# Kernel tuning notes

Hardware: AMD Instinct MI355X
Metric: run time of the kernel (lower is better)

The kernel has to match this reference:

```python
import jax, jax.numpy as jnp
import numpy as np

N_IN = 200000
N_OUT = 400000
K = 27          # 3x3x3 kernel offsets
P = 100000      # rulebook pairs per offset
C_IN = 32
C_OUT = 32


def setup_inputs() -> dict:
    key = jax.random.key(0)
    k1, k2, k3, k4, k5 = jax.random.split(key, 5)
    feats = jax.random.normal(k1, (N_IN, C_IN), dtype=jnp.float32)
    weight = jax.random.normal(k2, (K, C_IN, C_OUT), dtype=jnp.float32) * (1.0 / np.sqrt(C_IN * K))
    bias_param = jax.random.normal(k3, (C_OUT,), dtype=jnp.float32) * 0.01
    pairs_in = jax.random.randint(k4, (K, P), 0, N_IN, dtype=jnp.int64)
    pairs_out = jax.random.randint(k5, (K, P), 0, N_OUT, dtype=jnp.int64)
    return {
        "feats": feats,
        "weight": weight,
        "bias_param": bias_param,
        "pairs_in": pairs_in,
        "pairs_out": pairs_out,
        "n_out": N_OUT,
    }


def reference(feats, weight, bias_param, pairs_in, pairs_out, n_out):
    # Rulebook-based sparse inverse conv3d:
    #   1) gather input features per kernel offset  -> [K, P, C_in]
    #   2) per-offset GEMM with that offset's slice -> [K, P, C_out]
    #   3) scatter-add results into output voxels   -> [N_out, C_out]
    gathered = feats[pairs_in]                       # [K, P, C_in]
    vals = jnp.einsum('kpc,kco->kpo', gathered, weight)  # [K, P, C_out]
    out = jnp.zeros((n_out, vals.shape[-1]), dtype=feats.dtype)
    out = out.at[pairs_out.reshape(-1)].add(vals.reshape(-1, vals.shape[-1]))
    out = out + bias_param
    return out
```

## Files before the change

### kernel.cpp

```cpp
#include <hip/hip_runtime.h>

#define KK 27
#define PP 100000
#define C_IN 32
#define C_OUT 32
#define N_IN 200000
#define N_OUT 400000
#define PAIRS_PER_BLOCK 160

__global__ __launch_bounds__(256) void init_out_kernel(
    float4* __restrict__ out4, const float4* __restrict__ bias4) {
    int i = blockIdx.x * 256 + threadIdx.x;
    out4[i] = bias4[i & 7];
}

__global__ __launch_bounds__(256) void spconv_scatter_kernel(
    const float* __restrict__ feats,
    const float* __restrict__ weight,
    const int* __restrict__ pin,
    const int* __restrict__ pout,
    float* __restrict__ out)
{
    const int k   = blockIdx.y;
    const int c   = threadIdx.x & 31;
    const int grp = threadIdx.x >> 5;

    const float* w = weight + k * (C_IN * C_OUT) + c;
    float wcol[C_IN];
#pragma unroll
    for (int ci = 0; ci < C_IN; ++ci) wcol[ci] = w[ci * C_OUT];

    const int* pin_k  = pin  + k * PP;
    const int* pout_k = pout + k * PP;

    const int base = blockIdx.x * PAIRS_PER_BLOCK + grp;

#pragma unroll 4
    for (int i = 0; i < PAIRS_PER_BLOCK / 8; ++i) {
        const int p  = base + i * 8;
        const int ii = pin_k[p];
        const int io = pout_k[p];

        const float4* f4 = (const float4*)(feats + ii * 32);
        float acc = 0.0f;
#pragma unroll
        for (int j = 0; j < 8; ++j) {
            const float4 f = f4[j];
            acc = fmaf(f.x, wcol[4 * j + 0], acc);
            acc = fmaf(f.y, wcol[4 * j + 1], acc);
            acc = fmaf(f.z, wcol[4 * j + 2], acc);
            acc = fmaf(f.w, wcol[4 * j + 3], acc);
        }
        atomicAdd(out + io * 32 + c, acc);
    }
}

extern "C" void kernel_launch(void* const* d_in, const int* in_sizes, int n_in,
                              void* d_out, int out_size, void* d_ws, size_t ws_size,
                              hipStream_t stream) {
    const float* feats  = (const float*)d_in[0];
    const float* weight = (const float*)d_in[1];
    const float* bias   = (const float*)d_in[2];
    const int*   pin    = (const int*)d_in[3];
    const int*   pout   = (const int*)d_in[4];
    float*       out    = (float*)d_out;

    const int n_f4 = N_OUT * C_OUT / 4;
    init_out_kernel<<<n_f4 / 256, 256, 0, stream>>>(
        (float4*)out, (const float4*)bias);

    dim3 grid(PP / PAIRS_PER_BLOCK, KK);
    spconv_scatter_kernel<<<grid, 256, 0, stream>>>(
        feats, weight, pin, pout, out);
}
```

Baseline: 497.0 us.

## Partition output rows into XCD-local slices to localize scatter atomics

Each block now scans a chunk of pairs and processes only those whose output row falls in one of 16 row slices. Blocks are ordered so that round-robin dispatch sends each slice to a fixed XCD, keeping the atomic targets inside that XCD's L2. The change also switches to unsafeAtomicAdd, which lets the compiler emit hardware float atomics, and uses nontemporal loads for indices and features. The cost is that every pout index is read 16 times and the per-pair branch diverges within a wave.

Result: slower. 1.227 ms (+147.0%).

```diff
diff --git a/kernel.cpp b/kernel.cpp
--- a/kernel.cpp
+++ b/kernel.cpp
@@ -6,22 +6,40 @@
 #define C_OUT 32
 #define N_IN 200000
 #define N_OUT 400000
-#define PAIRS_PER_BLOCK 160
+
+#define SLICES 16
+#define ROWS_PER_SLICE (N_OUT / SLICES)
+#define XCDS 8
+#define CHUNK 4000
+#define CGRPS (PP / CHUNK)
+#define HALF_BLOCKS (XCDS * CGRPS * KK)
+#define TOTAL_BLOCKS (2 * HALF_BLOCKS)
+
+typedef int   vint4   __attribute__((ext_vector_type(4)));
+typedef float vfloat4 __attribute__((ext_vector_type(4)));
 
 __global__ __launch_bounds__(256) void init_out_kernel(
-    float4* __restrict__ out4, const float4* __restrict__ bias4) {
+    vfloat4* __restrict__ out4, const vfloat4* __restrict__ bias4) {
     int i = blockIdx.x * 256 + threadIdx.x;
     out4[i] = bias4[i & 7];
 }
 
-__global__ __launch_bounds__(256) void spconv_scatter_kernel(
+__global__ __launch_bounds__(256) void spconv_sliced_kernel(
     const float* __restrict__ feats,
     const float* __restrict__ weight,
     const int* __restrict__ pin,
     const int* __restrict__ pout,
     float* __restrict__ out)
 {
-    const int k   = blockIdx.y;
+    const int b    = blockIdx.x;
+    const int sub  = b / HALF_BLOCKS;
+    const int bb   = b % HALF_BLOCKS;
+    const int xslc = bb % XCDS;
+    const int rest = bb / XCDS;
+    const int cgrp = rest % CGRPS;
+    const int k    = rest / CGRPS;
+    const int r_lo = (xslc + XCDS * sub) * ROWS_PER_SLICE;
+
     const int c   = threadIdx.x & 31;
     const int grp = threadIdx.x >> 5;
 
@@ -33,25 +51,31 @@
     const int* pin_k  = pin  + k * PP;
     const int* pout_k = pout + k * PP;
 
-    const int base = blockIdx.x * PAIRS_PER_BLOCK + grp;
+    const int span = cgrp * CHUNK + grp * (CHUNK / 8);
+    const vint4* po4p = (const vint4*)(pout_k + span);
 
-#pragma unroll 4
-    for (int i = 0; i < PAIRS_PER_BLOCK / 8; ++i) {
-        const int p  = base + i * 8;
-        const int ii = pin_k[p];
-        const int io = pout_k[p];
+    for (int i4 = 0; i4 < CHUNK / 8 / 4; ++i4) {
+        const vint4 po4 = __builtin_nontemporal_load(po4p + i4);
+#pragma unroll
+        for (int j = 0; j < 4; ++j) {
+            const int io = po4[j];
+            if ((unsigned)(io - r_lo) < (unsigned)ROWS_PER_SLICE) {
+                const int p  = span + i4 * 4 + j;
+                const int ii = __builtin_nontemporal_load(pin_k + p);
 
-        const float4* f4 = (const float4*)(feats + ii * 32);
-        float acc = 0.0f;
+                const vfloat4* f4 = (const vfloat4*)(feats + ii * 32);
+                float acc = 0.0f;
 #pragma unroll
-        for (int j = 0; j < 8; ++j) {
-            const float4 f = f4[j];
-            acc = fmaf(f.x, wcol[4 * j + 0], acc);
-            acc = fmaf(f.y, wcol[4 * j + 1], acc);
-            acc = fmaf(f.z, wcol[4 * j + 2], acc);
-            acc = fmaf(f.w, wcol[4 * j + 3], acc);
+                for (int q = 0; q < 8; ++q) {
+                    const vfloat4 f = __builtin_nontemporal_load(f4 + q);
+                    acc = fmaf(f.x, wcol[4 * q + 0], acc);
+                    acc = fmaf(f.y, wcol[4 * q + 1], acc);
+                    acc = fmaf(f.z, wcol[4 * q + 2], acc);
+                    acc = fmaf(f.w, wcol[4 * q + 3], acc);
+                }
+                unsafeAtomicAdd(out + io * 32 + c, acc);
+            }
         }
-        atomicAdd(out + io * 32 + c, acc);
     }
 }
 
@@ -67,9 +91,8 @@
 
     const int n_f4 = N_OUT * C_OUT / 4;
     init_out_kernel<<<n_f4 / 256, 256, 0, stream>>>(
-        (float4*)out, (const float4*)bias);
+        (vfloat4*)out, (const vfloat4*)bias);
 
-    dim3 grid(PP / PAIRS_PER_BLOCK, KK);
-    spconv_scatter_kernel<<<grid, 256, 0, stream>>>(
+    spconv_sliced_kernel<<<TOTAL_BLOCKS, 256, 0, stream>>>(
         feats, weight, pin, pout, out);
 }
```

## Bucket rulebook pairs by output row block and accumulate in shared memory

Applied to the files above, without the earlier changes.

Replaces the global-atomic scatter with a counting-sort of all rulebook pairs into buckets of 128 output rows (count, column scan, base scan, scatter), then one block per bucket gathers features, applies the per-offset weights, accumulates with shared-memory atomics and writes each output row once with bias added. This removes global atomic traffic and the separate output init pass. In exchange it adds four preprocessing kernels with their own passes over the index arrays, a serial column-scan kernel, a single-block scan, and weight reloads whenever the offset changes within a bucket. Pair order inside a bucket is nondeterministic, so offsets may interleave and force frequent weight reloads.

New measurement: 643.1 us. 1.29x slower.

```diff
diff --git a/kernel.cpp b/kernel.cpp
--- a/kernel.cpp
+++ b/kernel.cpp
@@ -2,56 +2,196 @@
 
 #define KK 27
 #define PP 100000
+#define RTOT (KK * PP)
 #define C_IN 32
 #define C_OUT 32
 #define N_IN 200000
 #define N_OUT 400000
-#define PAIRS_PER_BLOCK 160
-
-__global__ __launch_bounds__(256) void init_out_kernel(
-    float4* __restrict__ out4, const float4* __restrict__ bias4) {
-    int i = blockIdx.x * 256 + threadIdx.x;
-    out4[i] = bias4[i & 7];
-}
-
-__global__ __launch_bounds__(256) void spconv_scatter_kernel(
+
+#define RPB 128
+#define NBUCK (N_OUT / RPB)
+#define NBLKA 450
+#define CHA (RTOT / NBLKA)
+
+typedef float vfloat4 __attribute__((ext_vector_type(4)));
+
+
+__global__ __launch_bounds__(256) void countA_kernel(
+    const int* __restrict__ pout, unsigned* __restrict__ C) {
+    __shared__ unsigned h[NBUCK];
+    const int t = threadIdx.x, blk = blockIdx.x;
+    for (int j = t; j < NBUCK; j += 256) h[j] = 0u;
+    __syncthreads();
+    const int g0 = blk * CHA;
+    for (int i = t; i < CHA; i += 256)
+        atomicAdd(&h[pout[g0 + i] >> 7], 1u);
+    __syncthreads();
+    unsigned* Crow = C + (size_t)blk * NBUCK;
+    for (int j = t; j < NBUCK; j += 256) Crow[j] = h[j];
+}
+
+__global__ __launch_bounds__(256) void scanCols_kernel(
+    unsigned* __restrict__ C, unsigned* __restrict__ T) {
+    const int b = blockIdx.x * 256 + threadIdx.x;
+    if (b >= NBUCK) return;
+    unsigned run = 0;
+    for (int blk = 0; blk < NBLKA; ++blk) {
+        const size_t idx = (size_t)blk * NBUCK + b;
+        const unsigned v = C[idx];
+        C[idx] = run;
+        run += v;
+    }
+    T[b] = run;
+}
+
+__global__ __launch_bounds__(1024) void scanBase_kernel(
+    const unsigned* __restrict__ T, unsigned* __restrict__ base) {
+    __shared__ unsigned ts[1024];
+    const int t = threadIdx.x;
+    const int i0 = t * 4;
+    unsigned v[4], s = 0;
+#pragma unroll
+    for (int j = 0; j < 4; ++j) {
+        v[j] = (i0 + j < NBUCK) ? T[i0 + j] : 0u;
+        s += v[j];
+    }
+    ts[t] = s;
+    __syncthreads();
+    for (int o = 1; o < 1024; o <<= 1) {
+        unsigned x = (t >= o) ? ts[t - o] : 0u;
+        __syncthreads();
+        ts[t] += x;
+        __syncthreads();
+    }
+    unsigned run = ts[t] - s;
+#pragma unroll
+    for (int j = 0; j < 4; ++j) {
+        if (i0 + j < NBUCK) base[i0 + j] = run;
+        run += v[j];
+    }
+    if (t == 0) base[NBUCK] = (unsigned)RTOT;
+}
+
+__global__ __launch_bounds__(256) void scatterA_kernel(
+    const int* __restrict__ pin, const int* __restrict__ pout,
+    const unsigned* __restrict__ C, const unsigned* __restrict__ base,
+    unsigned* __restrict__ bucket) {
+    __shared__ unsigned curs[NBUCK];
+    const int t = threadIdx.x, blk = blockIdx.x;
+    const unsigned* Prow = C + (size_t)blk * NBUCK;
+    for (int j = t; j < NBUCK; j += 256) curs[j] = base[j] + Prow[j];
+    __syncthreads();
+    const int g0 = blk * CHA;
+    for (int i = t; i < CHA; i += 256) {
+        const int g   = g0 + i;
+        const int row = pout[g];
+        const unsigned k  = (unsigned)g / PP;
+        const unsigned pk = (k << 25) | ((unsigned)(row & 127) << 18)
+                          | (unsigned)pin[g];
+        const unsigned pos = atomicAdd(&curs[row >> 7], 1u);
+        bucket[pos] = pk;
+    }
+}
+
+__global__ __launch_bounds__(256) void gather_accum_kernel(
     const float* __restrict__ feats,
     const float* __restrict__ weight,
-    const int* __restrict__ pin,
-    const int* __restrict__ pout,
+    const unsigned* __restrict__ base,
+    const unsigned* __restrict__ bucket,
+    const float* __restrict__ bias,
     float* __restrict__ out)
 {
-    const int k   = blockIdx.y;
-    const int c   = threadIdx.x & 31;
-    const int grp = threadIdx.x >> 5;
-
-    const float* w = weight + k * (C_IN * C_OUT) + c;
+    __shared__ float accum[RPB][C_OUT];
+    const int t = threadIdx.x, b = blockIdx.x;
+    const int c = t & 31, grp = t >> 5;
+
+    for (int j = t; j < RPB * C_OUT; j += 256) ((float*)accum)[j] = 0.0f;
+    __syncthreads();
+
+    const int s0  = (int)base[b];
+    const int len = (int)base[b + 1] - s0;
+    int e        = s0 + (len * grp) / 8;
+    const int ee = s0 + (len * (grp + 1)) / 8;
+
+    int kc = -1;
     float wcol[C_IN];
-#pragma unroll
-    for (int ci = 0; ci < C_IN; ++ci) wcol[ci] = w[ci * C_OUT];
-
-    const int* pin_k  = pin  + k * PP;
-    const int* pout_k = pout + k * PP;
-
-    const int base = blockIdx.x * PAIRS_PER_BLOCK + grp;
-
-#pragma unroll 4
-    for (int i = 0; i < PAIRS_PER_BLOCK / 8; ++i) {
-        const int p  = base + i * 8;
-        const int ii = pin_k[p];
-        const int io = pout_k[p];
-
-        const float4* f4 = (const float4*)(feats + ii * 32);
-        float acc = 0.0f;
+
+    for (; e + 1 < ee; e += 2) {
+        const unsigned pk0 = bucket[e];
+        const unsigned pk1 = bucket[e + 1];
+        const vfloat4* f0p = (const vfloat4*)(feats + (pk0 & 0x3FFFFu) * C_IN);
+        const vfloat4* f1p = (const vfloat4*)(feats + (pk1 & 0x3FFFFu) * C_IN);
+        vfloat4 f0[8], f1[8];
+#pragma unroll
+        for (int j = 0; j < 8; ++j) f0[j] = f0p[j];
+#pragma unroll
+        for (int j = 0; j < 8; ++j) f1[j] = f1p[j];
+
+        const int k0 = (int)(pk0 >> 25);
+        if (k0 != kc) {
+            kc = k0;
+            const float* w = weight + k0 * (C_IN * C_OUT) + c;
+#pragma unroll
+            for (int ci = 0; ci < C_IN; ++ci) wcol[ci] = w[ci * C_OUT];
+        }
+        float a0 = 0.0f;
 #pragma unroll
         for (int j = 0; j < 8; ++j) {
-            const float4 f = f4[j];
-            acc = fmaf(f.x, wcol[4 * j + 0], acc);
-            acc = fmaf(f.y, wcol[4 * j + 1], acc);
-            acc = fmaf(f.z, wcol[4 * j + 2], acc);
-            acc = fmaf(f.w, wcol[4 * j + 3], acc);
-        }
-        atomicAdd(out + io * 32 + c, acc);
+            a0 = fmaf(f0[j].x, wcol[4 * j + 0], a0);
+            a0 = fmaf(f0[j].y, wcol[4 * j + 1], a0);
+            a0 = fmaf(f0[j].z, wcol[4 * j + 2], a0);
+            a0 = fmaf(f0[j].w, wcol[4 * j + 3], a0);
+        }
+        atomicAdd(&accum[(pk0 >> 18) & 127][c], a0);
+
+        const int k1 = (int)(pk1 >> 25);
+        if (k1 != kc) {
+            kc = k1;
+            const float* w = weight + k1 * (C_IN * C_OUT) + c;
+#pragma unroll
+            for (int ci = 0; ci < C_IN; ++ci) wcol[ci] = w[ci * C_OUT];
+        }
+        float a1 = 0.0f;
+#pragma unroll
+        for (int j = 0; j < 8; ++j) {
+            a1 = fmaf(f1[j].x, wcol[4 * j + 0], a1);
+            a1 = fmaf(f1[j].y, wcol[4 * j + 1], a1);
+            a1 = fmaf(f1[j].z, wcol[4 * j + 2], a1);
+            a1 = fmaf(f1[j].w, wcol[4 * j + 3], a1);
+        }
+        atomicAdd(&accum[(pk1 >> 18) & 127][c], a1);
+    }
+    for (; e < ee; ++e) {
+        const unsigned pk = bucket[e];
+        const vfloat4* fp = (const vfloat4*)(feats + (pk & 0x3FFFFu) * C_IN);
+        vfloat4 f[8];
+#pragma unroll
+        for (int j = 0; j < 8; ++j) f[j] = fp[j];
+        const int k = (int)(pk >> 25);
+        if (k != kc) {
+            kc = k;
+            const float* w = weight + k * (C_IN * C_OUT) + c;
+#pragma unroll
+            for (int ci = 0; ci < C_IN; ++ci) wcol[ci] = w[ci * C_OUT];
+        }
+        float a = 0.0f;
+#pragma unroll
+        for (int j = 0; j < 8; ++j) {
+            a = fmaf(f[j].x, wcol[4 * j + 0], a);
+            a = fmaf(f[j].y, wcol[4 * j + 1], a);
+            a = fmaf(f[j].z, wcol[4 * j + 2], a);
+            a = fmaf(f[j].w, wcol[4 * j + 3], a);
+        }
+        atomicAdd(&accum[(pk >> 18) & 127][c], a);
+    }
+
+    __syncthreads();
+    const int R0 = b * RPB;
+    const float bv = bias[c];
+#pragma unroll
+    for (int j = 0; j < RPB / 8; ++j) {
+        const int r = grp + 8 * j;
+        out[(R0 + r) * C_OUT + c] = accum[r][c] + bv;
     }
 }
 
@@ -65,11 +205,15 @@
     const int*   pout   = (const int*)d_in[4];
     float*       out    = (float*)d_out;
 
-    const int n_f4 = N_OUT * C_OUT / 4;
-    init_out_kernel<<<n_f4 / 256, 256, 0, stream>>>(
-        (float4*)out, (const float4*)bias);
-
-    dim3 grid(PP / PAIRS_PER_BLOCK, KK);
-    spconv_scatter_kernel<<<grid, 256, 0, stream>>>(
-        feats, weight, pin, pout, out);
-}
+    unsigned* C      = (unsigned*)d_ws;
+    unsigned* T      = C + (size_t)NBLKA * NBUCK;
+    unsigned* base   = T + NBUCK;
+    unsigned* bucket = base + (NBUCK + 1);
+
+    countA_kernel  <<<NBLKA, 256, 0, stream>>>(pout, C);
+    scanCols_kernel<<<(NBUCK + 255) / 256, 256, 0, stream>>>(C, T);
+    scanBase_kernel<<<1, 1024, 0, stream>>>(T, base);
+    scatterA_kernel<<<NBLKA, 256, 0, stream>>>(pin, pout, C, base, bucket);
+    gather_accum_kernel<<<NBUCK, 256, 0, stream>>>(
+        feats, weight, base, bucket, bias, out);
+}
```
